# Kernel optimization log

Measured on AMD Instinct MI355X. Metric: run time of the kernel, lower is better.

The kernel has to match this reference:

```python
import jax, jax.numpy as jnp
import numpy as np

FACTOR = 2
LN_EPS = 1e-5


def _make_spatial_shapes():
    # 30 ragged tiles, all dims divisible by FACTOR; total tokens = 58368
    cycle = [(16, 16), (32, 32), (48, 48), (64, 64), (32, 64)]
    shapes = np.array([cycle[i % len(cycle)] for i in range(30)], dtype=np.int64)
    return shapes


def _unshuffle_index(spatial_shapes, factor):
    """Row-gather indices implementing per-tile pixel unshuffle.

    Returns int32 array (total_out_tokens, factor*factor): for each output
    (block) row, the factor^2 input rows whose features are concatenated.
    """
    ss = np.asarray(spatial_shapes)
    parts, off = [], 0
    for h, w in ss:
        h, w = int(h), int(w)
        if h == 0 or w == 0:
            continue
        a = (np.arange(h * w, dtype=np.int32)
             .reshape(h // factor, factor, w // factor, factor)
             .transpose(0, 2, 1, 3)
             .reshape(-1, factor * factor)) + off
        parts.append(a)
        off += h * w
    return np.concatenate(parts, axis=0)


def setup_inputs() -> dict:
    key = jax.random.key(0)
    ks = jax.random.split(key, 4)
    spatial_shapes = jnp.asarray(_make_spatial_shapes())
    total_tokens = int(np.sum(np.prod(_make_spatial_shapes(), axis=1)))  # 58368
    H = 1024                      # vision hidden size
    IC = H * FACTOR * FACTOR      # 4096 in_channels
    PH = 4096                     # projector hidden
    TH = 2048                     # text hidden
    return {
        "vision_features_packed": jax.random.normal(ks[0], (total_tokens, H), jnp.float32),
        "spatial_shapes": spatial_shapes,
        "ln_gamma": jnp.ones((IC,), jnp.float32),
        "ln_beta": jnp.zeros((IC,), jnp.float32),
        "w1": jax.random.normal(ks[1], (IC, PH), jnp.float32) * (IC ** -0.5),
        "b1": jnp.zeros((PH,), jnp.float32),
        "w2": jax.random.normal(ks[2], (PH, TH), jnp.float32) * (PH ** -0.5),
        "b2": jnp.zeros((TH,), jnp.float32),
    }


def reference(vision_features_packed, spatial_shapes, ln_gamma, ln_beta, w1, b1, w2, b2):
    H = vision_features_packed.shape[-1]
    idx = jnp.asarray(_unshuffle_index(spatial_shapes, FACTOR))  # (N_out, f*f)
    # single fused gather replacing the per-tile split/view/permute/cat loop
    unshuffled = vision_features_packed[idx].reshape(idx.shape[0], FACTOR * FACTOR * H)
    # LayerNorm over in_channels
    mu = jnp.mean(unshuffled, axis=-1, keepdims=True)
    var = jnp.var(unshuffled, axis=-1, keepdims=True)
    x = (unshuffled - mu) * jax.lax.rsqrt(var + LN_EPS) * ln_gamma + ln_beta
    # 2-layer MLP with exact GELU
    h = jax.nn.gelu(x @ w1 + b1, approximate=False)
    return h @ w2 + b2
```

## Files before the change

### kernel.cpp

```cpp
#include <hip/hip_runtime.h>
#include <hip/hip_bf16.h>

#define N_OUT 14592
#define HVIS 1024
#define IC 4096
#define PH 4096
#define TH 2048
#define NTILES 30
#define LN_EPS 1e-5f

typedef float f32x4 __attribute__((ext_vector_type(4)));
typedef __bf16 bf16x8 __attribute__((ext_vector_type(8)));
typedef unsigned short us8 __attribute__((ext_vector_type(8)));
typedef unsigned short us4 __attribute__((ext_vector_type(4)));

__device__ inline unsigned short f2bf(float x) {
    union { float f; unsigned u; } v; v.f = x;
    unsigned r = v.u + 0x7FFFu + ((v.u >> 16) & 1u);
    return (unsigned short)(r >> 16);
}
__device__ inline float bf2f(unsigned short h) {
    union { unsigned u; float f; } v; v.u = ((unsigned)h) << 16; return v.f;
}

__global__ void build_index(const int* __restrict__ ss_raw, int* __restrict__ idx) {
    __shared__ int t_w[NTILES], t_in[NTILES], t_out[NTILES + 1];
    if (threadIdx.x == 0) {
        int stride = (ss_raw[1] == 0) ? 2 : 1;
        int in_off = 0, out_off = 0;
        for (int t = 0; t < NTILES; ++t) {
            int h = ss_raw[(2 * t + 0) * stride];
            int w = ss_raw[(2 * t + 1) * stride];
            t_w[t] = w; t_in[t] = in_off; t_out[t] = out_off;
            in_off += h * w;
            out_off += (h / 2) * (w / 2);
        }
        t_out[NTILES] = out_off;
    }
    __syncthreads();
    for (int r = blockIdx.x * blockDim.x + threadIdx.x; r < N_OUT;
         r += gridDim.x * blockDim.x) {
        int t = 0;
        while (t + 1 < NTILES && r >= t_out[t + 1]) ++t;
        int local = r - t_out[t];
        int w = t_w[t];
        int wb = w >> 1;
        int i0 = local / wb;
        int i2 = local - i0 * wb;
        int base = t_in[t] + (2 * i0) * w + 2 * i2;
        idx[4 * r + 0] = base;
        idx[4 * r + 1] = base + 1;
        idx[4 * r + 2] = base + w;
        idx[4 * r + 3] = base + w + 1;
    }
}

__global__ void row_stats(const float* __restrict__ vis, const int* __restrict__ idx,
                          float* __restrict__ mu, float* __restrict__ rsig) {
    const int r = blockIdx.x;
    const int tid = threadIdx.x;
    int toks[4];
#pragma unroll
    for (int j = 0; j < 4; ++j) toks[j] = idx[4 * r + j];
    float s = 0.f, ss = 0.f;
#pragma unroll
    for (int i = 0; i < 4; ++i) {
        int slot = tid + i * 256;
        int j = slot >> 8;
        int c4 = slot & 255;
        const f32x4 v = *(const f32x4*)(vis + (size_t)toks[j] * HVIS + c4 * 4);
        s += v[0] + v[1] + v[2] + v[3];
        ss += v[0] * v[0] + v[1] * v[1] + v[2] * v[2] + v[3] * v[3];
    }
#pragma unroll
    for (int off = 32; off > 0; off >>= 1) {
        s += __shfl_down(s, off);
        ss += __shfl_down(ss, off);
    }
    __shared__ float ps[4], pss[4];
    int w = tid >> 6;
    if ((tid & 63) == 0) { ps[w] = s; pss[w] = ss; }
    __syncthreads();
    if (tid == 0) {
        float S = ps[0] + ps[1] + ps[2] + ps[3];
        float SS = pss[0] + pss[1] + pss[2] + pss[3];
        float m = S * (1.f / (float)IC);
        float v = SS * (1.f / (float)IC) - m * m;
        mu[r] = m;
        rsig[r] = rsqrtf(v + LN_EPS);
    }
}

__global__ void bias_fold(const float* __restrict__ b1, const float* __restrict__ beta,
                          const float* __restrict__ w1, float* __restrict__ b1p) {
    __shared__ float part[8][32];
    const int n0 = blockIdx.x * 32;
    const int c = threadIdx.x & 31, ph = threadIdx.x >> 5;
    float acc = 0.f;
    for (int k = ph; k < IC; k += 8)
        acc += beta[k] * w1[(size_t)k * PH + n0 + c];
    part[ph][c] = acc;
    __syncthreads();
    if (threadIdx.x < 32) {
        float s = b1[n0 + c];
#pragma unroll
        for (int i = 0; i < 8; ++i) s += part[i][c];
        b1p[n0 + c] = s;
    }
}

template <int APPLY_GAMMA>
__global__ void transpose_split(const float* __restrict__ src, const float* __restrict__ gamma,
                                unsigned short* __restrict__ dhi, unsigned short* __restrict__ dlo,
                                int K, int N) {
    __shared__ float t[32][33];
    const int k0 = blockIdx.y * 32, n0 = blockIdx.x * 32;
    const int tid = threadIdx.x;
    {
        const int r = tid >> 3, c4 = (tid & 7) * 4;
        f32x4 v = *(const f32x4*)(src + (size_t)(k0 + r) * N + n0 + c4);
        if (APPLY_GAMMA) { const float g = gamma[k0 + r]; v = v * g; }
        t[r][c4 + 0] = v[0]; t[r][c4 + 1] = v[1]; t[r][c4 + 2] = v[2]; t[r][c4 + 3] = v[3];
    }
    __syncthreads();
    const int nr = tid >> 3, kc = (tid & 7) * 4;
    us4 h, l;
#pragma unroll
    for (int i = 0; i < 4; ++i) {
        const float x = t[kc + i][nr];
        const unsigned short hb = f2bf(x);
        h[i] = hb; l[i] = f2bf(x - bf2f(hb));
    }
    *(us4*)(dhi + (size_t)(n0 + nr) * K + k0 + kc) = h;
    *(us4*)(dlo + (size_t)(n0 + nr) * K + k0 + kc) = l;
}

template <int MODE>
__global__ __launch_bounds__(256, 2) void gemm_split(
    const float* __restrict__ vis, const int* __restrict__ idx,
    const float* __restrict__ mu, const float* __restrict__ rsig,
    const unsigned short* __restrict__ Ahi, const unsigned short* __restrict__ Alo,
    const unsigned short* __restrict__ Bhi, const unsigned short* __restrict__ Blo,
    const float* __restrict__ bias,
    unsigned short* __restrict__ outHi, unsigned short* __restrict__ outLo,
    float* __restrict__ outF, int Ncols) {
    __shared__ unsigned short lds[2][4][4096];

    const int tid = threadIdx.x;
    const int lane = tid & 63;
    const int wv = tid >> 6;
    const int wr = wv >> 1, wc = wv & 1;

    const int nbx = gridDim.x;
    const int d = blockIdx.y * nbx + blockIdx.x;
    const int q = (nbx * 114) >> 3;
    const int swz = (d & 7) * q + (d >> 3);
    const int bn = swz / 114;
    const int bm = swz - bn * 114;

    const int sr = tid >> 1;
    const int sh = tid & 1;

    float s_mu = 0.f, s_rs = 0.f;
    if constexpr (MODE == 0) {
        s_mu = mu[bm * 128 + sr];
        s_rs = rsig[bm * 128 + sr];
    }

    const size_t KEL = 4096;
    f32x4 ra0, ra1, ra2, ra3;
    f32x4 rb0, rb1, rb2, rb3;

    auto LOAD = [&](int kt) {
        const int k0 = kt * 32;
        if constexpr (MODE == 0) {
            const int j = k0 >> 10;
            const int tok = idx[4 * (bm * 128 + sr) + j];
            const float* p = vis + (size_t)tok * HVIS + (k0 & 1023) + sh * 16;
            ra0 = *(const f32x4*)(p + 0);  ra1 = *(const f32x4*)(p + 4);
            ra2 = *(const f32x4*)(p + 8);  ra3 = *(const f32x4*)(p + 12);
        } else {
            const unsigned short* pa = Ahi + (size_t)(bm * 128 + sr) * KEL + k0 + sh * 16;
            const unsigned short* pl = Alo + (size_t)(bm * 128 + sr) * KEL + k0 + sh * 16;
            ra0 = *(const f32x4*)(pa); ra1 = *(const f32x4*)(pa + 8);
            ra2 = *(const f32x4*)(pl); ra3 = *(const f32x4*)(pl + 8);
        }
        const unsigned short* pb = Bhi + (size_t)(bn * 128 + sr) * KEL + k0 + sh * 16;
        const unsigned short* pq = Blo + (size_t)(bn * 128 + sr) * KEL + k0 + sh * 16;
        rb0 = *(const f32x4*)(pb); rb1 = *(const f32x4*)(pb + 8);
        rb2 = *(const f32x4*)(pq); rb3 = *(const f32x4*)(pq + 8);
    };

    const int dbase = (sr >> 4) * 512 + (sr & 15) * 8;
    const int c0 = 2 * sh, c1 = 2 * sh + 1;

    auto STORE = [&](int buf) {
        if constexpr (MODE == 0) {
            float v[16];
            *(f32x4*)&v[0] = ra0; *(f32x4*)&v[4] = ra1;
            *(f32x4*)&v[8] = ra2; *(f32x4*)&v[12] = ra3;
            us8 h0, h1, l0, l1;
#pragma unroll
            for (int i = 0; i < 8; ++i) {
                const float x = (v[i] - s_mu) * s_rs;
                const unsigned short hb = f2bf(x);
                h0[i] = hb; l0[i] = f2bf(x - bf2f(hb));
                const float y = (v[8 + i] - s_mu) * s_rs;
                const unsigned short hb2 = f2bf(y);
                h1[i] = hb2; l1[i] = f2bf(y - bf2f(hb2));
            }
            *(us8*)&lds[buf][0][dbase + c0 * 128] = h0;
            *(us8*)&lds[buf][0][dbase + c1 * 128] = h1;
            *(us8*)&lds[buf][1][dbase + c0 * 128] = l0;
            *(us8*)&lds[buf][1][dbase + c1 * 128] = l1;
        } else {
            *(f32x4*)&lds[buf][0][dbase + c0 * 128] = ra0;
            *(f32x4*)&lds[buf][0][dbase + c1 * 128] = ra1;
            *(f32x4*)&lds[buf][1][dbase + c0 * 128] = ra2;
            *(f32x4*)&lds[buf][1][dbase + c1 * 128] = ra3;
        }
        *(f32x4*)&lds[buf][2][dbase + c0 * 128] = rb0;
        *(f32x4*)&lds[buf][2][dbase + c1 * 128] = rb1;
        *(f32x4*)&lds[buf][3][dbase + c0 * 128] = rb2;
        *(f32x4*)&lds[buf][3][dbase + c1 * 128] = rb3;
    };

    f32x4 acc[4][4];
#pragma unroll
    for (int i = 0; i < 4; ++i)
#pragma unroll
        for (int j = 0; j < 4; ++j) acc[i][j] = (f32x4)0.f;

    const int foff = (lane >> 4) * 128 + (lane & 15) * 8;

    LOAD(0);
    STORE(0);
    __syncthreads();

    const int NT = 128;
    for (int kt = 0; kt < NT; ++kt) {
        const int cur = kt & 1;
        if (kt + 1 < NT) LOAD(kt + 1);

        bf16x8 bh[4], bl[4];
#pragma unroll
        for (int ni = 0; ni < 4; ++ni) {
            bh[ni] = *(const bf16x8*)&lds[cur][2][(wc * 4 + ni) * 512 + foff];
            bl[ni] = *(const bf16x8*)&lds[cur][3][(wc * 4 + ni) * 512 + foff];
        }
#pragma unroll
        for (int mi = 0; mi < 4; ++mi) {
            const bf16x8 ah = *(const bf16x8*)&lds[cur][0][(wr * 4 + mi) * 512 + foff];
            const bf16x8 al = *(const bf16x8*)&lds[cur][1][(wr * 4 + mi) * 512 + foff];
#pragma unroll
            for (int ni = 0; ni < 4; ++ni) {
                acc[mi][ni] = __builtin_amdgcn_mfma_f32_16x16x32_bf16(ah, bh[ni], acc[mi][ni], 0, 0, 0);
                acc[mi][ni] = __builtin_amdgcn_mfma_f32_16x16x32_bf16(ah, bl[ni], acc[mi][ni], 0, 0, 0);
                acc[mi][ni] = __builtin_amdgcn_mfma_f32_16x16x32_bf16(al, bh[ni], acc[mi][ni], 0, 0, 0);
            }
        }
        if (kt + 1 < NT) STORE(cur ^ 1);
        __syncthreads();
    }

    const int er = bm * 128 + wr * 64 + (lane >> 4) * 4;
    const int ec = bn * 128 + wc * 64 + (lane & 15);
    const float inv_sqrt2 = 0.70710678118654752f;
#pragma unroll
    for (int ni = 0; ni < 4; ++ni) {
        const int c = ec + ni * 16;
        const float bia = bias[c];
#pragma unroll
        for (int mi = 0; mi < 4; ++mi) {
#pragma unroll
            for (int j = 0; j < 4; ++j) {
                const int r = er + mi * 16 + j;
                const float o = acc[mi][ni][j] + bia;
                if constexpr (MODE == 0) {
                    const float g = 0.5f * o * (1.f + erff(o * inv_sqrt2));
                    const unsigned short hb = f2bf(g);
                    outHi[(size_t)r * PH + c] = hb;
                    outLo[(size_t)r * PH + c] = f2bf(g - bf2f(hb));
                } else {
                    outF[(size_t)r * Ncols + c] = o;
                }
            }
        }
    }
}

extern "C" void kernel_launch(void* const* d_in, const int* in_sizes, int n_in,
                              void* d_out, int out_size, void* d_ws, size_t ws_size,
                              hipStream_t stream) {
    const float* vis   = (const float*)d_in[0];
    const int*   ss    = (const int*)d_in[1];
    const float* gamma = (const float*)d_in[2];
    const float* beta  = (const float*)d_in[3];
    const float* w1    = (const float*)d_in[4];
    const float* b1    = (const float*)d_in[5];
    const float* w2    = (const float*)d_in[6];
    const float* b2    = (const float*)d_in[7];
    float* out = (float*)d_out;

    char* ws = (char*)d_ws;
    const size_t MiB = 1024 * 1024;
    int*            idx   = (int*)ws;
    float*          mu    = (float*)(ws + 256 * 1024);
    float*          rsig  = (float*)(ws + 320 * 1024);
    float*          b1p   = (float*)(ws + 384 * 1024);
    unsigned short* w1hi  = (unsigned short*)(ws + 1 * MiB);
    unsigned short* w1lo  = (unsigned short*)(ws + 33 * MiB);
    unsigned short* w2hi  = (unsigned short*)(ws + 65 * MiB);
    unsigned short* w2lo  = (unsigned short*)(ws + 81 * MiB);
    unsigned short* Hhi   = (unsigned short*)(ws + 97 * MiB);
    unsigned short* Hlo   = (unsigned short*)(ws + 212 * MiB);

    build_index<<<57, 256, 0, stream>>>(ss, idx);
    row_stats<<<N_OUT, 256, 0, stream>>>(vis, idx, mu, rsig);
    bias_fold<<<PH / 32, 256, 0, stream>>>(b1, beta, w1, b1p);
    transpose_split<1><<<dim3(PH / 32, IC / 32), 256, 0, stream>>>(w1, gamma, w1hi, w1lo, IC, PH);
    transpose_split<0><<<dim3(TH / 32, PH / 32), 256, 0, stream>>>(w2, nullptr, w2hi, w2lo, PH, TH);

    gemm_split<0><<<dim3(PH / 128, N_OUT / 128), 256, 0, stream>>>(
        vis, idx, mu, rsig, nullptr, nullptr, w1hi, w1lo, b1p, Hhi, Hlo, nullptr, PH);
    gemm_split<1><<<dim3(TH / 128, N_OUT / 128), 256, 0, stream>>>(
        nullptr, nullptr, nullptr, nullptr, Hhi, Hlo, w2hi, w2lo, b2, nullptr, nullptr, out, TH);
}
```

Before: 3.687 ms.

## Single-buffer GEMM LDS with XOR swizzle, raise occupancy, prematerialize normalized X

The GEMM kernel moves from double-buffered to single-buffered LDS, with an extra barrier per K step. This cuts LDS use so launch bounds can rise to 4 blocks per CU. It also adds an XOR swizzle on the LDS store and fragment-read offsets to reduce bank conflicts. When the workspace is large enough, a new prep_x kernel gathers, layer-normalizes and splits the activations into bf16 hi/lo once, so the first GEMM reads contiguous bf16 instead of gathering fp32 and converting per tile. The cost is an extra activation buffer in memory, one more barrier per step, and less overlap between loads and MFMA.

```diff
diff --git a/kernel.cpp b/kernel.cpp
--- a/kernel.cpp
+++ b/kernel.cpp
@@ -8,6 +8,7 @@
 #define TH 2048
 #define NTILES 30
 #define LN_EPS 1e-5f
+#define NBM 114
 
 typedef float f32x4 __attribute__((ext_vector_type(4)));
 typedef __bf16 bf16x8 __attribute__((ext_vector_type(8)));
@@ -91,6 +92,53 @@
     }
 }
 
+__global__ void prep_x(const float* __restrict__ vis, const int* __restrict__ idx,
+                       unsigned short* __restrict__ Xhi, unsigned short* __restrict__ Xlo) {
+    const int r = blockIdx.x;
+    const int tid = threadIdx.x;
+    const int tok = idx[4 * r + (tid >> 6)];
+    const float* p = vis + (size_t)tok * HVIS + (tid & 63) * 16;
+    f32x4 v0 = *(const f32x4*)(p + 0);
+    f32x4 v1 = *(const f32x4*)(p + 4);
+    f32x4 v2 = *(const f32x4*)(p + 8);
+    f32x4 v3 = *(const f32x4*)(p + 12);
+
+    float s = (v0[0]+v0[1]+v0[2]+v0[3]) + (v1[0]+v1[1]+v1[2]+v1[3])
+            + (v2[0]+v2[1]+v2[2]+v2[3]) + (v3[0]+v3[1]+v3[2]+v3[3]);
+    float ss = v0[0]*v0[0]+v0[1]*v0[1]+v0[2]*v0[2]+v0[3]*v0[3]
+             + v1[0]*v1[0]+v1[1]*v1[1]+v1[2]*v1[2]+v1[3]*v1[3]
+             + v2[0]*v2[0]+v2[1]*v2[1]+v2[2]*v2[2]+v2[3]*v2[3]
+             + v3[0]*v3[0]+v3[1]*v3[1]+v3[2]*v3[2]+v3[3]*v3[3];
+#pragma unroll
+    for (int off = 32; off > 0; off >>= 1) {
+        s += __shfl_down(s, off);
+        ss += __shfl_down(ss, off);
+    }
+    __shared__ float ps[4], pss[4];
+    if ((tid & 63) == 0) { ps[tid >> 6] = s; pss[tid >> 6] = ss; }
+    __syncthreads();
+    const float S = ps[0] + ps[1] + ps[2] + ps[3];
+    const float SS = pss[0] + pss[1] + pss[2] + pss[3];
+    const float m = S * (1.f / (float)IC);
+    const float rs = rsqrtf(SS * (1.f / (float)IC) - m * m + LN_EPS);
+
+    float v[16];
+    *(f32x4*)&v[0] = v0; *(f32x4*)&v[4] = v1; *(f32x4*)&v[8] = v2; *(f32x4*)&v[12] = v3;
+    us8 h0, h1, l0, l1;
+#pragma unroll
+    for (int i = 0; i < 8; ++i) {
+        const float x = (v[i] - m) * rs;
+        const unsigned short hb = f2bf(x);
+        h0[i] = hb; l0[i] = f2bf(x - bf2f(hb));
+        const float y = (v[8 + i] - m) * rs;
+        const unsigned short hb2 = f2bf(y);
+        h1[i] = hb2; l1[i] = f2bf(y - bf2f(hb2));
+    }
+    const size_t o = (size_t)r * IC + tid * 16;
+    *(us8*)(Xhi + o) = h0; *(us8*)(Xhi + o + 8) = h1;
+    *(us8*)(Xlo + o) = l0; *(us8*)(Xlo + o + 8) = l1;
+}
+
 __global__ void bias_fold(const float* __restrict__ b1, const float* __restrict__ beta,
                           const float* __restrict__ w1, float* __restrict__ b1p) {
     __shared__ float part[8][32];
@@ -135,8 +183,8 @@
     *(us4*)(dlo + (size_t)(n0 + nr) * K + k0 + kc) = l;
 }
 
-template <int MODE>
-__global__ __launch_bounds__(256, 2) void gemm_split(
+template <int AMODE, int EPI>
+__global__ __launch_bounds__(256, 4) void gemm_split(
     const float* __restrict__ vis, const int* __restrict__ idx,
     const float* __restrict__ mu, const float* __restrict__ rsig,
     const unsigned short* __restrict__ Ahi, const unsigned short* __restrict__ Alo,
@@ -144,7 +192,7 @@
     const float* __restrict__ bias,
     unsigned short* __restrict__ outHi, unsigned short* __restrict__ outLo,
     float* __restrict__ outF, int Ncols) {
-    __shared__ unsigned short lds[2][4][4096];
+    __shared__ unsigned short lds[4][4096];
 
     const int tid = threadIdx.x;
     const int lane = tid & 63;
@@ -153,16 +201,18 @@
 
     const int nbx = gridDim.x;
     const int d = blockIdx.y * nbx + blockIdx.x;
-    const int q = (nbx * 114) >> 3;
+    const int q = (nbx * NBM) >> 3;
     const int swz = (d & 7) * q + (d >> 3);
-    const int bn = swz / 114;
-    const int bm = swz - bn * 114;
+    const int bn = swz / NBM;
+    const int bm = swz - bn * NBM;
 
     const int sr = tid >> 1;
     const int sh = tid & 1;
+    const int sg = sr >> 4, srr = sr & 15;
+    const int stbase = sg * 512 + (2 * sh) * 128 + ((srr ^ (sh << 2)) * 8);
 
     float s_mu = 0.f, s_rs = 0.f;
-    if constexpr (MODE == 0) {
+    if constexpr (AMODE == 0) {
         s_mu = mu[bm * 128 + sr];
         s_rs = rsig[bm * 128 + sr];
     }
@@ -173,9 +223,8 @@
 
     auto LOAD = [&](int kt) {
         const int k0 = kt * 32;
-        if constexpr (MODE == 0) {
-            const int j = k0 >> 10;
-            const int tok = idx[4 * (bm * 128 + sr) + j];
+        if constexpr (AMODE == 0) {
+            const int tok = idx[4 * (bm * 128 + sr) + (k0 >> 10)];
             const float* p = vis + (size_t)tok * HVIS + (k0 & 1023) + sh * 16;
             ra0 = *(const f32x4*)(p + 0);  ra1 = *(const f32x4*)(p + 4);
             ra2 = *(const f32x4*)(p + 8);  ra3 = *(const f32x4*)(p + 12);
@@ -191,11 +240,8 @@
         rb2 = *(const f32x4*)(pq); rb3 = *(const f32x4*)(pq + 8);
     };
 
-    const int dbase = (sr >> 4) * 512 + (sr & 15) * 8;
-    const int c0 = 2 * sh, c1 = 2 * sh + 1;
-
-    auto STORE = [&](int buf) {
-        if constexpr (MODE == 0) {
+    auto STORE = [&]() {
+        if constexpr (AMODE == 0) {
             float v[16];
             *(f32x4*)&v[0] = ra0; *(f32x4*)&v[4] = ra1;
             *(f32x4*)&v[8] = ra2; *(f32x4*)&v[12] = ra3;
@@ -209,20 +255,14 @@
                 const unsigned short hb2 = f2bf(y);
                 h1[i] = hb2; l1[i] = f2bf(y - bf2f(hb2));
             }
-            *(us8*)&lds[buf][0][dbase + c0 * 128] = h0;
-            *(us8*)&lds[buf][0][dbase + c1 * 128] = h1;
-            *(us8*)&lds[buf][1][dbase + c0 * 128] = l0;
-            *(us8*)&lds[buf][1][dbase + c1 * 128] = l1;
+            *(us8*)&lds[0][stbase] = h0;  *(us8*)&lds[0][stbase + 128] = h1;
+            *(us8*)&lds[1][stbase] = l0;  *(us8*)&lds[1][stbase + 128] = l1;
         } else {
-            *(f32x4*)&lds[buf][0][dbase + c0 * 128] = ra0;
-            *(f32x4*)&lds[buf][0][dbase + c1 * 128] = ra1;
-            *(f32x4*)&lds[buf][1][dbase + c0 * 128] = ra2;
-            *(f32x4*)&lds[buf][1][dbase + c1 * 128] = ra3;
-        }
-        *(f32x4*)&lds[buf][2][dbase + c0 * 128] = rb0;
-        *(f32x4*)&lds[buf][2][dbase + c1 * 128] = rb1;
-        *(f32x4*)&lds[buf][3][dbase + c0 * 128] = rb2;
-        *(f32x4*)&lds[buf][3][dbase + c1 * 128] = rb3;
+            *(f32x4*)&lds[0][stbase] = ra0; *(f32x4*)&lds[0][stbase + 128] = ra1;
+            *(f32x4*)&lds[1][stbase] = ra2; *(f32x4*)&lds[1][stbase + 128] = ra3;
+        }
+        *(f32x4*)&lds[2][stbase] = rb0; *(f32x4*)&lds[2][stbase + 128] = rb1;
+        *(f32x4*)&lds[3][stbase] = rb2; *(f32x4*)&lds[3][stbase + 128] = rb3;
     };
 
     f32x4 acc[4][4];
@@ -231,27 +271,27 @@
 #pragma unroll
         for (int j = 0; j < 4; ++j) acc[i][j] = (f32x4)0.f;
 
-    const int foff = (lane >> 4) * 128 + (lane & 15) * 8;
+    const int fc = lane >> 4, fr = lane & 15;
+    const int foff = fc * 128 + ((fr ^ ((fc >> 1) & 1) * 4) * 8);
 
     LOAD(0);
-    STORE(0);
+    STORE();
     __syncthreads();
 
     const int NT = 128;
     for (int kt = 0; kt < NT; ++kt) {
-        const int cur = kt & 1;
         if (kt + 1 < NT) LOAD(kt + 1);
 
         bf16x8 bh[4], bl[4];
 #pragma unroll
         for (int ni = 0; ni < 4; ++ni) {
-            bh[ni] = *(const bf16x8*)&lds[cur][2][(wc * 4 + ni) * 512 + foff];
-            bl[ni] = *(const bf16x8*)&lds[cur][3][(wc * 4 + ni) * 512 + foff];
+            bh[ni] = *(const bf16x8*)&lds[2][(wc * 4 + ni) * 512 + foff];
+            bl[ni] = *(const bf16x8*)&lds[3][(wc * 4 + ni) * 512 + foff];
         }
 #pragma unroll
         for (int mi = 0; mi < 4; ++mi) {
-            const bf16x8 ah = *(const bf16x8*)&lds[cur][0][(wr * 4 + mi) * 512 + foff];
-            const bf16x8 al = *(const bf16x8*)&lds[cur][1][(wr * 4 + mi) * 512 + foff];
+            const bf16x8 ah = *(const bf16x8*)&lds[0][(wr * 4 + mi) * 512 + foff];
+            const bf16x8 al = *(const bf16x8*)&lds[1][(wr * 4 + mi) * 512 + foff];
 #pragma unroll
             for (int ni = 0; ni < 4; ++ni) {
                 acc[mi][ni] = __builtin_amdgcn_mfma_f32_16x16x32_bf16(ah, bh[ni], acc[mi][ni], 0, 0, 0);
@@ -259,8 +299,11 @@
                 acc[mi][ni] = __builtin_amdgcn_mfma_f32_16x16x32_bf16(al, bh[ni], acc[mi][ni], 0, 0, 0);
             }
         }
-        if (kt + 1 < NT) STORE(cur ^ 1);
         __syncthreads();
+        if (kt + 1 < NT) {
+            STORE();
+            __syncthreads();
+        }
     }
 
     const int er = bm * 128 + wr * 64 + (lane >> 4) * 4;
@@ -276,11 +319,11 @@
             for (int j = 0; j < 4; ++j) {
                 const int r = er + mi * 16 + j;
                 const float o = acc[mi][ni][j] + bia;
-                if constexpr (MODE == 0) {
+                if constexpr (EPI == 0) {
                     const float g = 0.5f * o * (1.f + erff(o * inv_sqrt2));
                     const unsigned short hb = f2bf(g);
-                    outHi[(size_t)r * PH + c] = hb;
-                    outLo[(size_t)r * PH + c] = f2bf(g - bf2f(hb));
+                    outHi[(size_t)r * Ncols + c] = hb;
+                    outLo[(size_t)r * Ncols + c] = f2bf(g - bf2f(hb));
                 } else {
                     outF[(size_t)r * Ncols + c] = o;
                 }
@@ -312,17 +355,31 @@
     unsigned short* w1lo  = (unsigned short*)(ws + 33 * MiB);
     unsigned short* w2hi  = (unsigned short*)(ws + 65 * MiB);
     unsigned short* w2lo  = (unsigned short*)(ws + 81 * MiB);
-    unsigned short* Hhi   = (unsigned short*)(ws + 97 * MiB);
-    unsigned short* Hlo   = (unsigned short*)(ws + 212 * MiB);
 
     build_index<<<57, 256, 0, stream>>>(ss, idx);
-    row_stats<<<N_OUT, 256, 0, stream>>>(vis, idx, mu, rsig);
     bias_fold<<<PH / 32, 256, 0, stream>>>(b1, beta, w1, b1p);
     transpose_split<1><<<dim3(PH / 32, IC / 32), 256, 0, stream>>>(w1, gamma, w1hi, w1lo, IC, PH);
     transpose_split<0><<<dim3(TH / 32, PH / 32), 256, 0, stream>>>(w2, nullptr, w2hi, w2lo, PH, TH);
 
-    gemm_split<0><<<dim3(PH / 128, N_OUT / 128), 256, 0, stream>>>(
-        vis, idx, mu, rsig, nullptr, nullptr, w1hi, w1lo, b1p, Hhi, Hlo, nullptr, PH);
-    gemm_split<1><<<dim3(TH / 128, N_OUT / 128), 256, 0, stream>>>(
-        nullptr, nullptr, nullptr, nullptr, Hhi, Hlo, w2hi, w2lo, b2, nullptr, nullptr, out, TH);
-}
+    if (ws_size >= 560 * MiB) {
+        unsigned short* Xhi = (unsigned short*)(ws + 97 * MiB);
+        unsigned short* Xlo = (unsigned short*)(ws + 211 * MiB);
+        unsigned short* Hhi = (unsigned short*)(ws + 325 * MiB);
+        unsigned short* Hlo = (unsigned short*)(ws + 439 * MiB);
+
+        prep_x<<<N_OUT, 256, 0, stream>>>(vis, idx, Xhi, Xlo);
+        gemm_split<1, 0><<<dim3(PH / 128, NBM), 256, 0, stream>>>(
+            nullptr, nullptr, nullptr, nullptr, Xhi, Xlo, w1hi, w1lo, b1p, Hhi, Hlo, nullptr, PH);
+        gemm_split<1, 1><<<dim3(TH / 128, NBM), 256, 0, stream>>>(
+            nullptr, nullptr, nullptr, nullptr, Hhi, Hlo, w2hi, w2lo, b2, nullptr, nullptr, out, TH);
+    } else {
+        unsigned short* Hhi = (unsigned short*)(ws + 97 * MiB);
+        unsigned short* Hlo = (unsigned short*)(ws + 212 * MiB);
+
+        row_stats<<<N_OUT, 256, 0, stream>>>(vis, idx, mu, rsig);
+        gemm_split<0, 0><<<dim3(PH / 128, NBM), 256, 0, stream>>>(
+            vis, idx, mu, rsig, nullptr, nullptr, w1hi, w1lo, b1p, Hhi, Hlo, nullptr, PH);
+        gemm_split<1, 1><<<dim3(TH / 128, NBM), 256, 0, stream>>>(
+            nullptr, nullptr, nullptr, nullptr, Hhi, Hlo, w2hi, w2lo, b2, nullptr, nullptr, out, TH);
+    }
+}
```

After: 3.723 ms. About the same (+1.0%).
